# Optimization experiments

Measured on AMD Instinct MI355X. Metric: run time of the kernel, lower is better.

## Reference

```python
import jax, jax.numpy as jnp
import numpy as np

N, D, H, OUT, L = 4096, 127, 128, 3, 2
SIM_THRESH = 0.9
BN_EPS = 1e-5


def setup_inputs() -> dict:
    key = jax.random.key(0)
    ks = jax.random.split(key, 10)
    s = 1.0 / np.sqrt(H)
    x_now = jax.random.normal(ks[0], (N, D), dtype=jnp.float32)
    sat_type = jax.random.randint(ks[1], (N,), 0, 6, dtype=jnp.int64)
    # SAGEConv per layer: lin_l (neighbor aggr, with bias) and lin_r (root, no bias)
    Wl = jax.random.normal(ks[2], (L, H, H), dtype=jnp.float32) * s
    bl = jnp.zeros((L, H), dtype=jnp.float32)
    Wr = jax.random.normal(ks[3], (L, H, H), dtype=jnp.float32) * s
    gamma = jnp.ones((H,), dtype=jnp.float32)
    beta = jnp.zeros((H,), dtype=jnp.float32)
    Wo = jax.random.normal(ks[4], (OUT, H), dtype=jnp.float32) * s
    bo = jnp.zeros((OUT,), dtype=jnp.float32)
    return {"x_now": x_now, "sat_type": sat_type, "Wl": Wl, "bl": bl,
            "Wr": Wr, "gamma": gamma, "beta": beta, "Wo": Wo, "bo": bo}


def _forward(x_now, sat_type, Wl, bl, Wr, gamma, beta, Wo, bo):
    n = x_now.shape[0]
    # build_graph, h_prev=None branch: ppr = x_now[:, 0]
    x = jnp.concatenate([x_now[:, :1], x_now], axis=1)  # [N, H] with H = D+1
    # pairwise cosine similarity on first 4 features (F.normalize, eps=1e-12)
    f = x[:, :4]
    fn = f / jnp.maximum(jnp.linalg.norm(f, axis=1, keepdims=True), 1e-12)
    cos_sim = fn @ fn.T  # [N, N]
    same = sat_type[:, None] == sat_type[None, :]
    mask = (same | (cos_sim > SIM_THRESH)) & ~jnp.eye(n, dtype=bool)
    A = mask.astype(x.dtype)  # symmetric adjacency (dense form of edge list)
    deg = jnp.maximum(A.sum(axis=1, keepdims=True), 1.0)  # mean-aggr denom; isolated -> 0
    h = x
    for l in range(L):  # SAGEConv: lin_l(mean_j x_j) + lin_r(x_i), then ReLU
        m = (A @ h) / deg
        h = jax.nn.relu(m @ Wl[l].T + bl[l] + h @ Wr[l].T)
    # BatchNorm over nodes (training-mode batch stats, biased variance)
    mu = h.mean(axis=0)
    var = h.var(axis=0)
    h = (h - mu) / jnp.sqrt(var + BN_EPS) * gamma + beta
    out = h @ Wo.T + bo
    return h, out


def reference(x_now, sat_type, Wl, bl, Wr, gamma, beta, Wo, bo):
    return _forward(x_now, sat_type, Wl, bl, Wr, gamma, beta, Wo, bo)
```

## Files before the change

### kernel.cpp

```cpp
#include <hip/hip_runtime.h>
#include <hip/hip_bf16.h>
#include <math.h>

#define NN 4096
#define DD 127
#define HH 128
#define OUTD 3
#define NTYPES 6
#define SIM_THRESH 0.9f
#define BN_EPS 1e-5f
#define MROW 4
#define NREP 8
#define LMAXH 256

typedef unsigned short ushortT;

static __device__ inline ushortT f2bf(float f) {
    unsigned u = __float_as_uint(f);
    unsigned r = (u + 0x7fffu + ((u >> 16) & 1u)) >> 16;
    return (ushortT)r;
}

__global__ __launch_bounds__(256) void prep(
    const float* __restrict__ x_now, const int* __restrict__ sat,
    const float* __restrict__ Wl, const float* __restrict__ Wr,
    float* __restrict__ WT, float* __restrict__ x, ushortT* __restrict__ xbf,
    float4* __restrict__ fn, int* __restrict__ cnt, float* __restrict__ S0rep)
{
    int t = threadIdx.x;
    if (blockIdx.x < 32) {
        int m = blockIdx.x >> 3;
        int p = blockIdx.x & 7;
        const float* src = ((m < 2) ? (Wl + m * 16384) : (Wr + (m - 2) * 16384))
                           + p * 16 * 128;
        float* dst = WT + m * 16384 + p * 16;
        __shared__ float lds[16][129];
        #pragma unroll
        for (int it = 0; it < 8; ++it) {
            int lin = it * 256 + t;
            int o = lin >> 7, k = lin & 127;
            lds[o][k] = src[lin];
        }
        __syncthreads();
        #pragma unroll
        for (int it = 0; it < 8; ++it) {
            int lin = it * 256 + t;
            int k = lin >> 4, oo = lin & 15;
            dst[k * 128 + oo] = lds[oo][k];
        }
        return;
    }

    int sb = blockIdx.x - 32;
    int base = sb * 16;
    int rep = sb & (NREP - 1);
    __shared__ int stypes[16];
    int myti = -1;
    if (t < 16) {
        int row = base + t;
        int ti = sat[row]; ti = min(max(ti, 0), NTYPES - 1);
        stypes[t] = ti; myti = ti;
        const float* rp = x_now + (size_t)row * DD;
        float f0 = rp[0], f2 = rp[1], f3 = rp[2];
        float nrm = fmaxf(sqrtf(2.f * f0 * f0 + f2 * f2 + f3 * f3), 1e-12f);
        float inv = 1.f / nrm;
        fn[row] = make_float4(f0 * inv, f0 * inv, f2 * inv, f3 * inv);
    }
    #pragma unroll
    for (int it = 0; it < 8; ++it) {
        int lin = it * 256 + t;
        int rl = lin >> 7, col = lin & 127;
        int row = base + rl;
        const float* rp = x_now + (size_t)row * DD;
        float v = (col == 0) ? rp[0] : rp[col - 1];
        x[(size_t)row * HH + col] = v;
        xbf[(size_t)row * HH + col] = f2bf(v);
    }
    __syncthreads();
    if (t < 64) {
        #pragma unroll
        for (int tt = 0; tt < NTYPES; ++tt) {
            unsigned long long m = __ballot(myti == tt);
            if (t == 0) {
                int c = __popcll(m);
                if (c) atomicAdd(&cnt[rep * NTYPES + tt], c);
            }
        }
    }
    if (t < 128) {
        float acc[NTYPES] = {0.f, 0.f, 0.f, 0.f, 0.f, 0.f};
        for (int r = 0; r < 16; ++r) {
            float v = x[(size_t)(base + r) * HH + t];
            int tt = stypes[r];
            #pragma unroll
            for (int q = 0; q < NTYPES; ++q) acc[q] += (tt == q) ? v : 0.f;
        }
        #pragma unroll
        for (int q = 0; q < NTYPES; ++q)
            atomicAdd(&S0rep[(rep * NTYPES + q) * HH + t], acc[q]);
    }
}

__global__ __launch_bounds__(256) void build_mask(
    const float4* __restrict__ fn, const int* __restrict__ sat,
    const int* __restrict__ cnt, unsigned* __restrict__ mask,
    float* __restrict__ deg)
{
    int i0 = blockIdx.x * MROW;
    int t = threadIdx.x;
    int w = t & 127;
    int half = t >> 7;
    float4 fi[MROW];
    int ti[MROW];
    #pragma unroll
    for (int r = 0; r < MROW; ++r) {
        fi[r] = fn[i0 + r];
        int tt = sat[i0 + r];
        ti[r] = min(max(tt, 0), NTYPES - 1);
    }
    unsigned word[MROW] = {0, 0, 0, 0};
    int bbase = half * 16;
    for (int bb = 0; bb < 16; ++bb) {
        int b = bbase + bb;
        int j = b * 128 + w;
        float4 fj = fn[j];
        int tj = sat[j];
        #pragma unroll
        for (int r = 0; r < MROW; ++r) {
            float dot = fi[r].x * fj.x + fi[r].y * fj.y
                      + fi[r].z * fj.z + fi[r].w * fj.w;
            if (tj != ti[r] && dot > SIM_THRESH) word[r] |= (1u << b);
        }
    }
    __shared__ unsigned wpart[MROW][128];
    if (half == 1) {
        #pragma unroll
        for (int r = 0; r < MROW; ++r) wpart[r][w] = word[r];
    }
    __syncthreads();
    __shared__ int wt[2][MROW];
    if (half == 0) {
        int pcs[MROW];
        #pragma unroll
        for (int r = 0; r < MROW; ++r) {
            unsigned full = word[r] | wpart[r][w];
            mask[(size_t)(i0 + r) * 128 + w] = full;
            pcs[r] = __popc(full);
        }
        int lane = w & 63, wv2 = w >> 6;
        for (int s = 32; s; s >>= 1) {
            #pragma unroll
            for (int r = 0; r < MROW; ++r) pcs[r] += __shfl_down(pcs[r], s);
        }
        if (lane == 0) {
            #pragma unroll
            for (int r = 0; r < MROW; ++r) wt[wv2][r] = pcs[r];
        }
    }
    __syncthreads();
    if (t < MROW) {
        int r = t;
        int ctot = 0;
        #pragma unroll
        for (int rr = 0; rr < NREP; ++rr) ctot += cnt[rr * NTYPES + ti[r]];
        float d = (float)(ctot - 1 + wt[0][r] + wt[1][r]);
        deg[i0 + r] = fmaxf(d, 1.0f);
    }
}

template <int MODE>
__global__ __launch_bounds__(256, 8) void layer_kernel(
    const float* __restrict__ h, const ushortT* __restrict__ hbf,
    const unsigned* __restrict__ mask,
    const float* __restrict__ deg, const float* __restrict__ S, int nrepS,
    const int* __restrict__ sat,
    const float* __restrict__ WTl, const float* __restrict__ bl,
    const float* __restrict__ WTr, float* __restrict__ hout,
    ushortT* __restrict__ houtbf,
    float* __restrict__ acc0, float* __restrict__ acc1)
{
    int t = threadIdx.x;
    int wv = t >> 6;
    int lane = t & 63;
    int r  = wv >> 1;
    int hf = wv & 1;
    int i0 = blockIdx.x * 2;
    int i = i0 + r;

    __shared__ ushortT list[4][LMAXH];
    __shared__ __align__(16) float hs[2][HH];
    __shared__ __align__(16) float ms[2][HH];
    __shared__ __align__(16) float part[4][HH];
    __shared__ int tarr[2];

    if (t < 2) {
        int tt = sat[i0 + t];
        tarr[t] = min(max(tt, 0), NTYPES - 1);
    }

    int widx = hf * 64 + lane;
    unsigned word = mask[(size_t)i * 128 + widx];
    int pc = __popc(word);
    int x = pc;
    for (int s = 1; s < 64; s <<= 1) {
        int v = __shfl_up(x, s);
        if (lane >= s) x += v;
    }
    int ncnt = __shfl(x, 63);
    int ofs = x - pc;
    unsigned ww = word;
    while (ww) {
        int b = __ffs(ww) - 1; ww &= ww - 1;
        list[wv][ofs++] = (ushortT)(b * 128 + widx);
    }
    if (hf == 0)
        ((float2*)hs[r])[lane] = ((const float2*)(h + (size_t)i * HH))[lane];

    int q = lane >> 4;
    int c = lane & 15;
    const uint4* __restrict__ hb4 = (const uint4*)hbf;
    float acc[8] = {0.f, 0.f, 0.f, 0.f, 0.f, 0.f, 0.f, 0.f};
#define BFACC(vv)                                                         \
    {                                                                     \
        acc[0] += __uint_as_float((vv).x << 16);                          \
        acc[1] += __uint_as_float((vv).x & 0xffff0000u);                  \
        acc[2] += __uint_as_float((vv).y << 16);                          \
        acc[3] += __uint_as_float((vv).y & 0xffff0000u);                  \
        acc[4] += __uint_as_float((vv).z << 16);                          \
        acc[5] += __uint_as_float((vv).z & 0xffff0000u);                  \
        acc[6] += __uint_as_float((vv).w << 16);                          \
        acc[7] += __uint_as_float((vv).w & 0xffff0000u);                  \
    }
    int g = 0;
    for (; g + 24 <= ncnt; g += 24) {
        int j0 = list[wv][g + q];
        int j1 = list[wv][g + 4 + q];
        int j2 = list[wv][g + 8 + q];
        int j3 = list[wv][g + 12 + q];
        int j4 = list[wv][g + 16 + q];
        int j5 = list[wv][g + 20 + q];
        uint4 v0 = hb4[j0 * 16 + c];
        uint4 v1 = hb4[j1 * 16 + c];
        uint4 v2 = hb4[j2 * 16 + c];
        uint4 v3 = hb4[j3 * 16 + c];
        uint4 v4 = hb4[j4 * 16 + c];
        uint4 v5 = hb4[j5 * 16 + c];
        BFACC(v0); BFACC(v1); BFACC(v2); BFACC(v3); BFACC(v4); BFACC(v5);
    }
    for (; g + 4 <= ncnt; g += 4) {
        int j0 = list[wv][g + q];
        uint4 v0 = hb4[j0 * 16 + c];
        BFACC(v0);
    }
    if (q < ncnt - g) {
        int j0 = list[wv][g + q];
        uint4 v0 = hb4[j0 * 16 + c];
        BFACC(v0);
    }
#undef BFACC
    #pragma unroll
    for (int d = 0; d < 8; ++d) {
        acc[d] += __shfl_down(acc[d], 32);
        acc[d] += __shfl_down(acc[d], 16);
    }
    if (lane < 16) {
        float4 p0 = {acc[0], acc[1], acc[2], acc[3]};
        float4 p1 = {acc[4], acc[5], acc[6], acc[7]};
        ((float4*)part[wv])[c * 2] = p0;
        ((float4*)part[wv])[c * 2 + 1] = p1;
    }
    __syncthreads();

    if (hf == 0 && lane < 32) {
        int cc = lane;
        float4 p0 = ((const float4*)part[wv])[cc];
        float4 p1 = ((const float4*)part[wv + 1])[cc];
        int ti = tarr[r];
        float rdeg = 1.f / deg[i];
        float4 hv = ((const float4*)hs[r])[cc];
        float4 Sv = {0.f, 0.f, 0.f, 0.f};
        for (int rr = 0; rr < nrepS; ++rr) {
            float4 sv = ((const float4*)S)[(rr * NTYPES + ti) * 32 + cc];
            Sv.x += sv.x; Sv.y += sv.y; Sv.z += sv.z; Sv.w += sv.w;
        }
        float4 m;
        m.x = (Sv.x - hv.x + p0.x + p1.x) * rdeg;
        m.y = (Sv.y - hv.y + p0.y + p1.y) * rdeg;
        m.z = (Sv.z - hv.z + p0.z + p1.z) * rdeg;
        m.w = (Sv.w - hv.w + p0.w + p1.w) * rdeg;
        ((float4*)ms[r])[cc] = m;
    }
    __syncthreads();

    int c4 = hf * 16 + (lane & 15);
    int kh = lane >> 4;
    const float4* __restrict__ WTl4 = (const float4*)WTl;
    const float4* __restrict__ WTr4 = (const float4*)WTr;
    const float* msr = ms[r];
    const float* hsr = hs[r];
    int kbase = kh * 32;
    float4 macc = {0.f, 0.f, 0.f, 0.f};
    #pragma unroll 4
    for (int kk = 0; kk < 32; ++kk) {
        int k = kbase + kk;
        float4 wl = WTl4[k * 32 + c4];
        float4 wr = WTr4[k * 32 + c4];
        float mk = msr[k];
        float hk = hsr[k];
        macc.x += mk * wl.x + hk * wr.x;
        macc.y += mk * wl.y + hk * wr.y;
        macc.z += mk * wl.z + hk * wr.z;
        macc.w += mk * wl.w + hk * wr.w;
    }
    macc.x += __shfl_down(macc.x, 32);
    macc.y += __shfl_down(macc.y, 32);
    macc.z += __shfl_down(macc.z, 32);
    macc.w += __shfl_down(macc.w, 32);
    macc.x += __shfl_down(macc.x, 16);
    macc.y += __shfl_down(macc.y, 16);
    macc.z += __shfl_down(macc.z, 16);
    macc.w += __shfl_down(macc.w, 16);
    if (lane < 16) {
        float4 bv = ((const float4*)bl)[c4];
        float4 o4;
        o4.x = fmaxf(macc.x + bv.x, 0.f);
        o4.y = fmaxf(macc.y + bv.y, 0.f);
        o4.z = fmaxf(macc.z + bv.z, 0.f);
        o4.w = fmaxf(macc.w + bv.w, 0.f);
        ((float4*)(hout + (size_t)i * HH))[c4] = o4;
        if (MODE == 1) {
            ushort4 b4;
            b4.x = f2bf(o4.x); b4.y = f2bf(o4.y);
            b4.z = f2bf(o4.z); b4.w = f2bf(o4.w);
            ((ushort4*)(houtbf + (size_t)i * HH))[c4] = b4;
        }
        ((float4*)part[r])[c4] = o4;
    }
    __syncthreads();

    int rep = blockIdx.x & (NREP - 1);
    if (MODE == 1) {
        if (t < HH) {
            #pragma unroll
            for (int rr = 0; rr < 2; ++rr)
                atomicAdd(&acc0[(rep * NTYPES + tarr[rr]) * HH + t], part[rr][t]);
        }
    } else {
        if (t < HH) {
            float s = 0.f, s2 = 0.f;
            #pragma unroll
            for (int rr = 0; rr < 2; ++rr) {
                float v = part[rr][t];
                s += v; s2 += v * v;
            }
            atomicAdd(&acc0[rep * HH + t], s);
            atomicAdd(&acc1[rep * HH + t], s2);
        }
    }
}

__global__ __launch_bounds__(256) void finalize(
    const float* __restrict__ h, const float* __restrict__ musum8,
    const float* __restrict__ varsum8, const float* __restrict__ gamma,
    const float* __restrict__ beta, const float* __restrict__ Wo,
    const float* __restrict__ bo, float* __restrict__ out_h,
    float* __restrict__ out_o)
{
    int t = threadIdx.x;
    int wv = t >> 6;
    int lane = t & 63;
    int i = blockIdx.x * 4 + wv;

    float2 mus = {0.f, 0.f}, vas = {0.f, 0.f};
    #pragma unroll
    for (int r = 0; r < NREP; ++r) {
        float2 a = ((const float2*)(musum8 + r * HH))[lane];
        float2 b = ((const float2*)(varsum8 + r * HH))[lane];
        mus.x += a.x; mus.y += a.y;
        vas.x += b.x; vas.y += b.y;
    }
    float2 ga  = ((const float2*)gamma)[lane];
    float2 be  = ((const float2*)beta)[lane];
    float mu0 = mus.x * (1.f / NN), mu1 = mus.y * (1.f / NN);
    float v0 = vas.x * (1.f / NN) - mu0 * mu0;
    float v1 = vas.y * (1.f / NN) - mu1 * mu1;
    float sc0 = ga.x / sqrtf(v0 + BN_EPS), sc1 = ga.y / sqrtf(v1 + BN_EPS);
    float sh0 = be.x - mu0 * sc0, sh1 = be.y - mu1 * sc1;

    float2 hv = ((const float2*)(h + (size_t)i * HH))[lane];
    float2 hb;
    hb.x = hv.x * sc0 + sh0;
    hb.y = hv.y * sc1 + sh1;
    ((float2*)(out_h + (size_t)i * HH))[lane] = hb;

    float2 w0 = ((const float2*)Wo)[lane];
    float2 w1 = ((const float2*)(Wo + HH))[lane];
    float2 w2 = ((const float2*)(Wo + 2 * HH))[lane];
    float p0 = hb.x * w0.x + hb.y * w0.y;
    float p1 = hb.x * w1.x + hb.y * w1.y;
    float p2 = hb.x * w2.x + hb.y * w2.y;
    for (int s = 32; s; s >>= 1) {
        p0 += __shfl_down(p0, s);
        p1 += __shfl_down(p1, s);
        p2 += __shfl_down(p2, s);
    }
    if (lane == 0) {
        out_o[(size_t)i * OUTD + 0] = p0 + bo[0];
        out_o[(size_t)i * OUTD + 1] = p1 + bo[1];
        out_o[(size_t)i * OUTD + 2] = p2 + bo[2];
    }
}

extern "C" void kernel_launch(void* const* d_in, const int* in_sizes, int n_in,
                              void* d_out, int out_size, void* d_ws, size_t ws_size,
                              hipStream_t stream)
{
    (void)in_sizes; (void)n_in; (void)out_size; (void)ws_size;
    const float* x_now = (const float*)d_in[0];
    const int*   sat   = (const int*)d_in[1];
    const float* Wl    = (const float*)d_in[2];
    const float* bl    = (const float*)d_in[3];
    const float* Wr    = (const float*)d_in[4];
    const float* gamma = (const float*)d_in[5];
    const float* beta  = (const float*)d_in[6];
    const float* Wo    = (const float*)d_in[7];
    const float* bo    = (const float*)d_in[8];

    float* ws = (float*)d_ws;
    float* x0 = ws;
    float* h1 = x0 + (size_t)NN * HH;
    float* h2 = h1 + (size_t)NN * HH;
    float* WT = h2 + (size_t)NN * HH;
    ushortT* x0bf = (ushortT*)(WT + 65536);
    ushortT* h1bf = x0bf + (size_t)NN * HH;
    float4* fn = (float4*)(h1bf + (size_t)NN * HH);
    unsigned* mask = (unsigned*)((float*)fn + 4 * NN);
    float* deg = (float*)(mask + (size_t)NN * 128);
    int*   cnt   = (int*)(deg + NN);
    float* S0rep = (float*)(cnt + 64);
    float* S1rep = S0rep + NREP * NTYPES * HH;
    float* mu8   = S1rep + NREP * NTYPES * HH;
    float* var8  = mu8 + NREP * HH;

    size_t zero_bytes = (64 + 2 * NREP * NTYPES * HH + 2 * NREP * HH)
                        * sizeof(float);
    hipMemsetAsync(cnt, 0, zero_bytes, stream);

    prep<<<288, 256, 0, stream>>>(x_now, sat, Wl, Wr, WT, x0, x0bf, fn, cnt,
                                  S0rep);
    build_mask<<<NN / MROW, 256, 0, stream>>>(fn, sat, cnt, mask, deg);

    layer_kernel<1><<<NN / 2, 256, 0, stream>>>(
        x0, x0bf, mask, deg, S0rep, NREP, sat, WT, bl, WT + 32768, h1, h1bf,
        S1rep, nullptr);
    layer_kernel<2><<<NN / 2, 256, 0, stream>>>(
        h1, h1bf, mask, deg, S1rep, NREP, sat, WT + 16384, bl + HH, WT + 49152,
        h2, nullptr, mu8, var8);

    finalize<<<NN / 4, 256, 0, stream>>>(h2, mu8, var8, gamma, beta, Wo, bo,
                                         (float*)d_out, (float*)d_out + (size_t)NN * HH);
}
```

Before: 156.8 us.

## Split layer into gather and bf16 MFMA GEMM kernels

Each SAGE layer kernel is split in two. A gather kernel computes the mean-aggregated neighbor features and writes them as bf16. A separate GEMM kernel then uses 16x16x32 bf16 MFMA instructions on 16-row tiles to apply Wl and Wr together, replacing the per-row scalar fp32 matvec. Weights are converted to bf16 in prep instead of being transposed in fp32. This adds two kernel launches and a global round trip for the aggregated features, and the linear layers now run at bf16 precision, which risks accuracy.

```diff
diff --git a/kernel.cpp b/kernel.cpp
--- a/kernel.cpp
+++ b/kernel.cpp
@@ -14,6 +14,8 @@
 #define LMAXH 256
 
 typedef unsigned short ushortT;
+typedef __attribute__((ext_vector_type(8))) short short8;
+typedef __attribute__((ext_vector_type(4))) float f32x4;
 
 static __device__ inline ushortT f2bf(float f) {
     unsigned u = __float_as_uint(f);
@@ -24,34 +26,23 @@
 __global__ __launch_bounds__(256) void prep(
     const float* __restrict__ x_now, const int* __restrict__ sat,
     const float* __restrict__ Wl, const float* __restrict__ Wr,
-    float* __restrict__ WT, float* __restrict__ x, ushortT* __restrict__ xbf,
-    float4* __restrict__ fn, int* __restrict__ cnt, float* __restrict__ S0rep)
+    ushortT* __restrict__ Wbf, float* __restrict__ x,
+    ushortT* __restrict__ xbf, float4* __restrict__ fn,
+    int* __restrict__ cnt, float* __restrict__ S0rep)
 {
     int t = threadIdx.x;
-    if (blockIdx.x < 32) {
-        int m = blockIdx.x >> 3;
-        int p = blockIdx.x & 7;
-        const float* src = ((m < 2) ? (Wl + m * 16384) : (Wr + (m - 2) * 16384))
-                           + p * 16 * 128;
-        float* dst = WT + m * 16384 + p * 16;
-        __shared__ float lds[16][129];
-        #pragma unroll
-        for (int it = 0; it < 8; ++it) {
-            int lin = it * 256 + t;
-            int o = lin >> 7, k = lin & 127;
-            lds[o][k] = src[lin];
-        }
-        __syncthreads();
-        #pragma unroll
-        for (int it = 0; it < 8; ++it) {
-            int lin = it * 256 + t;
-            int k = lin >> 4, oo = lin & 15;
-            dst[k * 128 + oo] = lds[oo][k];
+    if (blockIdx.x < 8) {
+        int baseidx = blockIdx.x * 8192;
+        #pragma unroll
+        for (int it = 0; it < 32; ++it) {
+            int idx = baseidx + it * 256 + t;
+            float v = (idx < 32768) ? Wl[idx] : Wr[idx - 32768];
+            Wbf[idx] = f2bf(v);
         }
         return;
     }
 
-    int sb = blockIdx.x - 32;
+    int sb = blockIdx.x - 8;
     int base = sb * 16;
     int rep = sb & (NREP - 1);
     __shared__ int stypes[16];
@@ -168,16 +159,11 @@
     }
 }
 
-template <int MODE>
-__global__ __launch_bounds__(256, 8) void layer_kernel(
+__global__ __launch_bounds__(256, 8) void gather_kernel(
     const float* __restrict__ h, const ushortT* __restrict__ hbf,
-    const unsigned* __restrict__ mask,
-    const float* __restrict__ deg, const float* __restrict__ S, int nrepS,
-    const int* __restrict__ sat,
-    const float* __restrict__ WTl, const float* __restrict__ bl,
-    const float* __restrict__ WTr, float* __restrict__ hout,
-    ushortT* __restrict__ houtbf,
-    float* __restrict__ acc0, float* __restrict__ acc1)
+    const unsigned* __restrict__ mask, const float* __restrict__ deg,
+    const float* __restrict__ S, const int* __restrict__ sat,
+    ushortT* __restrict__ mbf)
 {
     int t = threadIdx.x;
     int wv = t >> 6;
@@ -189,7 +175,6 @@
 
     __shared__ ushortT list[4][LMAXH];
     __shared__ __align__(16) float hs[2][HH];
-    __shared__ __align__(16) float ms[2][HH];
     __shared__ __align__(16) float part[4][HH];
     __shared__ int tarr[2];
 
@@ -279,7 +264,8 @@
         float rdeg = 1.f / deg[i];
         float4 hv = ((const float4*)hs[r])[cc];
         float4 Sv = {0.f, 0.f, 0.f, 0.f};
-        for (int rr = 0; rr < nrepS; ++rr) {
+        #pragma unroll
+        for (int rr = 0; rr < NREP; ++rr) {
             float4 sv = ((const float4*)S)[(rr * NTYPES + ti) * 32 + cc];
             Sv.x += sv.x; Sv.y += sv.y; Sv.z += sv.z; Sv.w += sv.w;
         }
@@ -288,69 +274,94 @@
         m.y = (Sv.y - hv.y + p0.y + p1.y) * rdeg;
         m.z = (Sv.z - hv.z + p0.z + p1.z) * rdeg;
         m.w = (Sv.w - hv.w + p0.w + p1.w) * rdeg;
-        ((float4*)ms[r])[cc] = m;
+        ushort4 mb;
+        mb.x = f2bf(m.x); mb.y = f2bf(m.y);
+        mb.z = f2bf(m.z); mb.w = f2bf(m.w);
+        ((ushort4*)(mbf + (size_t)i * HH))[cc] = mb;
+    }
+}
+
+template <int MODE>
+__global__ __launch_bounds__(256) void gemm_kernel(
+    const ushortT* __restrict__ mbf, const ushortT* __restrict__ hbf,
+    const ushortT* __restrict__ Wlbf, const ushortT* __restrict__ Wrbf,
+    const float* __restrict__ bl, const int* __restrict__ sat,
+    float* __restrict__ hout, ushortT* __restrict__ houtbf,
+    float* __restrict__ acc0, float* __restrict__ acc1)
+{
+    int t = threadIdx.x;
+    int wv = t >> 6, lane = t & 63;
+    int p = lane & 15, q = lane >> 4;
+    int i0 = blockIdx.x * 16;
+
+    __shared__ float sh[16][129];
+    __shared__ int stypes[16];
+    if (t < 16) {
+        int tt = sat[i0 + t];
+        stypes[t] = min(max(tt, 0), NTYPES - 1);
+    }
+
+    const ushortT* arow_m = mbf + (size_t)(i0 + p) * HH + q * 8;
+    const ushortT* arow_h = hbf + (size_t)(i0 + p) * HH + q * 8;
+    short8 am[4], ah[4];
+    #pragma unroll
+    for (int s = 0; s < 4; ++s) {
+        am[s] = *(const short8*)(arow_m + s * 32);
+        ah[s] = *(const short8*)(arow_h + s * 32);
+    }
+
+    #pragma unroll
+    for (int nt = 0; nt < 2; ++nt) {
+        int n0 = (wv * 2 + nt) * 16;
+        const ushortT* brow_l = Wlbf + (size_t)(n0 + p) * HH + q * 8;
+        const ushortT* brow_r = Wrbf + (size_t)(n0 + p) * HH + q * 8;
+        f32x4 acc = {0.f, 0.f, 0.f, 0.f};
+        #pragma unroll
+        for (int s = 0; s < 4; ++s) {
+            short8 b = *(const short8*)(brow_l + s * 32);
+            acc = __builtin_amdgcn_mfma_f32_16x16x32_bf16(am[s], b, acc, 0, 0, 0);
+        }
+        #pragma unroll
+        for (int s = 0; s < 4; ++s) {
+            short8 b = *(const short8*)(brow_r + s * 32);
+            acc = __builtin_amdgcn_mfma_f32_16x16x32_bf16(ah[s], b, acc, 0, 0, 0);
+        }
+        int o = n0 + p;
+        float bv = bl[o];
+        #pragma unroll
+        for (int rg = 0; rg < 4; ++rg) {
+            float v = fmaxf(acc[rg] + bv, 0.f);
+            sh[q * 4 + rg][o] = v;
+        }
     }
     __syncthreads();
 
-    int c4 = hf * 16 + (lane & 15);
-    int kh = lane >> 4;
-    const float4* __restrict__ WTl4 = (const float4*)WTl;
-    const float4* __restrict__ WTr4 = (const float4*)WTr;
-    const float* msr = ms[r];
-    const float* hsr = hs[r];
-    int kbase = kh * 32;
-    float4 macc = {0.f, 0.f, 0.f, 0.f};
-    #pragma unroll 4
-    for (int kk = 0; kk < 32; ++kk) {
-        int k = kbase + kk;
-        float4 wl = WTl4[k * 32 + c4];
-        float4 wr = WTr4[k * 32 + c4];
-        float mk = msr[k];
-        float hk = hsr[k];
-        macc.x += mk * wl.x + hk * wr.x;
-        macc.y += mk * wl.y + hk * wr.y;
-        macc.z += mk * wl.z + hk * wr.z;
-        macc.w += mk * wl.w + hk * wr.w;
-    }
-    macc.x += __shfl_down(macc.x, 32);
-    macc.y += __shfl_down(macc.y, 32);
-    macc.z += __shfl_down(macc.z, 32);
-    macc.w += __shfl_down(macc.w, 32);
-    macc.x += __shfl_down(macc.x, 16);
-    macc.y += __shfl_down(macc.y, 16);
-    macc.z += __shfl_down(macc.z, 16);
-    macc.w += __shfl_down(macc.w, 16);
-    if (lane < 16) {
-        float4 bv = ((const float4*)bl)[c4];
-        float4 o4;
-        o4.x = fmaxf(macc.x + bv.x, 0.f);
-        o4.y = fmaxf(macc.y + bv.y, 0.f);
-        o4.z = fmaxf(macc.z + bv.z, 0.f);
-        o4.w = fmaxf(macc.w + bv.w, 0.f);
-        ((float4*)(hout + (size_t)i * HH))[c4] = o4;
+    #pragma unroll
+    for (int e = 0; e < 8; ++e) {
+        int lin = e * 256 + t;
+        int rr = lin >> 7, cc = lin & 127;
+        float v = sh[rr][cc];
+        hout[(size_t)i0 * HH + lin] = v;
+        if (MODE == 1) houtbf[(size_t)i0 * HH + lin] = f2bf(v);
+    }
+    int rep = blockIdx.x & (NREP - 1);
+    if (t < HH) {
         if (MODE == 1) {
-            ushort4 b4;
-            b4.x = f2bf(o4.x); b4.y = f2bf(o4.y);
-            b4.z = f2bf(o4.z); b4.w = f2bf(o4.w);
-            ((ushort4*)(houtbf + (size_t)i * HH))[c4] = b4;
-        }
-        ((float4*)part[r])[c4] = o4;
-    }
-    __syncthreads();
-
-    int rep = blockIdx.x & (NREP - 1);
-    if (MODE == 1) {
-        if (t < HH) {
+            float accq[NTYPES] = {0.f, 0.f, 0.f, 0.f, 0.f, 0.f};
+            for (int r = 0; r < 16; ++r) {
+                float v = sh[r][t];
+                int tt = stypes[r];
+                #pragma unroll
+                for (int qq = 0; qq < NTYPES; ++qq)
+                    accq[qq] += (tt == qq) ? v : 0.f;
+            }
             #pragma unroll
-            for (int rr = 0; rr < 2; ++rr)
-                atomicAdd(&acc0[(rep * NTYPES + tarr[rr]) * HH + t], part[rr][t]);
-        }
-    } else {
-        if (t < HH) {
+            for (int qq = 0; qq < NTYPES; ++qq)
+                atomicAdd(&acc0[(rep * NTYPES + qq) * HH + t], accq[qq]);
+        } else {
             float s = 0.f, s2 = 0.f;
-            #pragma unroll
-            for (int rr = 0; rr < 2; ++rr) {
-                float v = part[rr][t];
+            for (int r = 0; r < 16; ++r) {
+                float v = sh[r][t];
                 s += v; s2 += v * v;
             }
             atomicAdd(&acc0[rep * HH + t], s);
@@ -430,10 +441,11 @@
     float* x0 = ws;
     float* h1 = x0 + (size_t)NN * HH;
     float* h2 = h1 + (size_t)NN * HH;
-    float* WT = h2 + (size_t)NN * HH;
-    ushortT* x0bf = (ushortT*)(WT + 65536);
+    ushortT* Wbf  = (ushortT*)(h2 + (size_t)NN * HH);
+    ushortT* x0bf = Wbf + 65536;
     ushortT* h1bf = x0bf + (size_t)NN * HH;
-    float4* fn = (float4*)(h1bf + (size_t)NN * HH);
+    ushortT* mbf  = h1bf + (size_t)NN * HH;
+    float4* fn = (float4*)(mbf + (size_t)NN * HH);
     unsigned* mask = (unsigned*)((float*)fn + 4 * NN);
     float* deg = (float*)(mask + (size_t)NN * 128);
     int*   cnt   = (int*)(deg + NN);
@@ -446,16 +458,20 @@
                         * sizeof(float);
     hipMemsetAsync(cnt, 0, zero_bytes, stream);
 
-    prep<<<288, 256, 0, stream>>>(x_now, sat, Wl, Wr, WT, x0, x0bf, fn, cnt,
+    prep<<<264, 256, 0, stream>>>(x_now, sat, Wl, Wr, Wbf, x0, x0bf, fn, cnt,
                                   S0rep);
     build_mask<<<NN / MROW, 256, 0, stream>>>(fn, sat, cnt, mask, deg);
 
-    layer_kernel<1><<<NN / 2, 256, 0, stream>>>(
-        x0, x0bf, mask, deg, S0rep, NREP, sat, WT, bl, WT + 32768, h1, h1bf,
-        S1rep, nullptr);
-    layer_kernel<2><<<NN / 2, 256, 0, stream>>>(
-        h1, h1bf, mask, deg, S1rep, NREP, sat, WT + 16384, bl + HH, WT + 49152,
-        h2, nullptr, mu8, var8);
+    gather_kernel<<<NN / 2, 256, 0, stream>>>(x0, x0bf, mask, deg, S0rep, sat,
+                                              mbf);
+    gemm_kernel<1><<<NN / 16, 256, 0, stream>>>(
+        mbf, x0bf, Wbf, Wbf + 32768, bl, sat, h1, h1bf, S1rep, nullptr);
+
+    gather_kernel<<<NN / 2, 256, 0, stream>>>(h1, h1bf, mask, deg, S1rep, sat,
+                                              mbf);
+    gemm_kernel<2><<<NN / 16, 256, 0, stream>>>(
+        mbf, h1bf, Wbf + 16384, Wbf + 49152, bl + HH, sat, h2, nullptr,
+        mu8, var8);
 
     finalize<<<NN / 4, 256, 0, stream>>>(h2, mu8, var8, gamma, beta, Wo, bo,
                                          (float*)d_out, (float*)d_out + (size_t)NN * HH);
```

Result: faster. 136.3 us, median of 2 (-13.1%).
